# Optimization experiments

Hardware: AMD Instinct MI355X
Metric: run time of the kernel (lower is better)

Reference implementation:

```python
import jax, jax.numpy as jnp
import numpy as np

B, N, E, H, FF = 2, 2048, 1024, 16, 4096
D = E // H  # head dim = 64
LN_EPS = 1e-5


def _layer_norm(x, gamma, beta):
    mu = jnp.mean(x, axis=-1, keepdims=True)
    var = jnp.var(x, axis=-1, keepdims=True)
    return (x - mu) * jax.lax.rsqrt(var + LN_EPS) * gamma + beta


def setup_inputs() -> dict:
    key = jax.random.key(0)
    ks = jax.random.split(key, 12)
    s = 0.02
    return {
        "x": jax.random.normal(ks[0], (B, N, 2), dtype=jnp.float32),
        "W_in": jax.random.normal(ks[1], (2, E), dtype=jnp.float32) * s,
        "b_in": jnp.zeros((E,), dtype=jnp.float32),
        "gamma": jnp.ones((E,), dtype=jnp.float32),
        "beta": jnp.zeros((E,), dtype=jnp.float32),
        "Wq": jax.random.normal(ks[2], (E, E), dtype=jnp.float32) * s,
        "bq": jnp.zeros((E,), dtype=jnp.float32),
        "Wk": jax.random.normal(ks[3], (E, E), dtype=jnp.float32) * s,
        "bk": jnp.zeros((E,), dtype=jnp.float32),
        "Wv": jax.random.normal(ks[4], (E, E), dtype=jnp.float32) * s,
        "bv": jnp.zeros((E,), dtype=jnp.float32),
        "Wo": jax.random.normal(ks[5], (E, E), dtype=jnp.float32) * s,
        "bo": jnp.zeros((E,), dtype=jnp.float32),
        "W1": jax.random.normal(ks[6], (E, FF), dtype=jnp.float32) * s,
        "b1": jnp.zeros((FF,), dtype=jnp.float32),
        "W2": jax.random.normal(ks[7], (FF, E), dtype=jnp.float32) * s,
        "b2": jnp.zeros((E,), dtype=jnp.float32),
    }


def reference(x, W_in, b_in, gamma, beta, Wq, bq, Wk, bk, Wv, bv, Wo, bo, W1, b1, W2, b2):
    # input projection: [B,N,2] -> [B,N,E]
    h = x @ W_in + b_in
    # pre-attention LayerNorm (shared params with pre-FFN LN in original)
    hL = _layer_norm(h, gamma, beta)

    def split_heads(t):  # [B,N,E] -> [B,H,N,D]
        return t.reshape(B, N, H, D).transpose(0, 2, 1, 3)

    q = split_heads(hL @ Wq + bq)
    k = split_heads(hL @ Wk + bk)
    v = split_heads(hL @ Wv + bv)

    # full score matrix, scaled by sqrt(emb_size) as in the original (NOT sqrt(head_dim))
    energy = jnp.einsum("bhqd,bhkd->bhqk", q, k)
    att = jax.nn.softmax(energy / jnp.sqrt(jnp.float32(E)), axis=-1)
    out = jnp.einsum("bhqk,bhkd->bhqd", att, v)
    out = out.transpose(0, 2, 1, 3).reshape(B, N, E)
    out = out @ Wo + bo

    h = h + out  # residual
    # FFN branch with SAME LayerNorm params
    f = _layer_norm(h, gamma, beta)
    f = jax.nn.gelu(f @ W1 + b1, approximate=False)
    f = f @ W2 + b2
    return h + f
```

## Files before the change

### kernel.cpp

```cpp
#include <hip/hip_runtime.h>
#include <hip/hip_bf16.h>
#include <stdint.h>

#define B_  2
#define N_  2048
#define E_  1024
#define H_  16
#define D_  64
#define FF_ 4096
#define M_  (B_ * N_)

typedef __bf16 bf16x8 __attribute__((ext_vector_type(8)));
typedef float  f32x4  __attribute__((ext_vector_type(4)));

__device__ __forceinline__ unsigned short f2bf(float x) {
  union { float f; uint32_t u; } v; v.f = x;
  v.u += 0x7fffu + ((v.u >> 16) & 1u);
  return (unsigned short)(v.u >> 16);
}

__device__ __forceinline__ void async16(void* lds, const void* g) {
  __builtin_amdgcn_global_load_lds(
      (const __attribute__((address_space(1))) uint32_t*)g,
      (__attribute__((address_space(3))) uint32_t*)lds, 16, 0, 0);
}

__global__ __launch_bounds__(256)
void k_transpose_bf16(const float* __restrict__ W, unsigned short* __restrict__ Wt,
                      int K, int N) {
  __shared__ float tile[64][65];
  const int n0 = blockIdx.x * 64, k0 = blockIdx.y * 64;
  const int t = threadIdx.x;
  const int c = t & 63, r4 = t >> 6;
#pragma unroll
  for (int i = 0; i < 16; ++i) {
    int r = r4 + i * 4;
    tile[r][c] = W[(size_t)(k0 + r) * N + n0 + c];
  }
  __syncthreads();
#pragma unroll
  for (int i = 0; i < 16; ++i) {
    int r = r4 + i * 4;
    Wt[(size_t)(n0 + r) * K + k0 + c] = f2bf(tile[c][r]);
  }
}

__global__ __launch_bounds__(256)
void k_inproj_ln(const float* __restrict__ x, const float* __restrict__ Win,
                 const float* __restrict__ bin, const float* __restrict__ gamma,
                 const float* __restrict__ beta, float* __restrict__ h,
                 unsigned short* __restrict__ hL) {
  const int m = blockIdx.x, t = threadIdx.x;
  const float x0 = x[m * 2], x1 = x[m * 2 + 1];
  float hv[4], s = 0.f, s2 = 0.f;
#pragma unroll
  for (int i = 0; i < 4; ++i) {
    int c = t + i * 256;
    float v = x0 * Win[c] + x1 * Win[E_ + c] + bin[c];
    hv[i] = v; s += v; s2 += v * v;
  }
#pragma unroll
  for (int off = 1; off < 64; off <<= 1) { s += __shfl_xor(s, off); s2 += __shfl_xor(s2, off); }
  __shared__ float ws1[4], ws2[4];
  const int w = t >> 6, lane = t & 63;
  if (lane == 0) { ws1[w] = s; ws2[w] = s2; }
  __syncthreads();
  s  = ws1[0] + ws1[1] + ws1[2] + ws1[3];
  s2 = ws2[0] + ws2[1] + ws2[2] + ws2[3];
  const float mu = s * (1.f / E_);
  const float var = s2 * (1.f / E_) - mu * mu;
  const float rs = 1.f / sqrtf(var + 1e-5f);
#pragma unroll
  for (int i = 0; i < 4; ++i) {
    int c = t + i * 256;
    h [(size_t)m * E_ + c] = hv[i];
    hL[(size_t)m * E_ + c] = f2bf((hv[i] - mu) * rs * gamma[c] + beta[c]);
  }
}

__global__ __launch_bounds__(256)
void k_ln(const float* __restrict__ h, const float* __restrict__ gamma,
          const float* __restrict__ beta, unsigned short* __restrict__ o) {
  const int m = blockIdx.x, t = threadIdx.x;
  const float4 v4 = *reinterpret_cast<const float4*>(&h[(size_t)m * E_ + t * 4]);
  float s = v4.x + v4.y + v4.z + v4.w;
  float s2 = v4.x * v4.x + v4.y * v4.y + v4.z * v4.z + v4.w * v4.w;
#pragma unroll
  for (int off = 1; off < 64; off <<= 1) { s += __shfl_xor(s, off); s2 += __shfl_xor(s2, off); }
  __shared__ float ws1[4], ws2[4];
  const int w = t >> 6, lane = t & 63;
  if (lane == 0) { ws1[w] = s; ws2[w] = s2; }
  __syncthreads();
  s  = ws1[0] + ws1[1] + ws1[2] + ws1[3];
  s2 = ws2[0] + ws2[1] + ws2[2] + ws2[3];
  const float mu = s * (1.f / E_);
  const float var = s2 * (1.f / E_) - mu * mu;
  const float rs = 1.f / sqrtf(var + 1e-5f);
  const float vv[4] = {v4.x, v4.y, v4.z, v4.w};
#pragma unroll
  for (int i = 0; i < 4; ++i) {
    int c = t * 4 + i;
    o[(size_t)m * E_ + c] = f2bf((vv[i] - mu) * rs * gamma[c] + beta[c]);
  }
}

template <bool OUT_BF16, bool GELU, bool RES>
__global__ __launch_bounds__(256, 2)
void k_gemm(const unsigned short* __restrict__ A, const unsigned short* __restrict__ Bt,
            const float* __restrict__ bias, const float* __restrict__ res,
            void* __restrict__ Cout, int M, int N, int K) {
  __shared__ unsigned short As[128 * 64];
  __shared__ unsigned short Bs[128 * 64];
  const int t = threadIdx.x, lane = t & 63, w = t >> 6;
  const int wr = w >> 1, wc = w & 1;
  const int row0 = blockIdx.y * 128, col0 = blockIdx.x * 128;
  const int lr = lane & 15, lk = (lane >> 4) * 8;

  f32x4 acc[4][4];
#pragma unroll
  for (int m = 0; m < 4; ++m)
#pragma unroll
    for (int n = 0; n < 4; ++n) acc[m][n] = f32x4{0.f, 0.f, 0.f, 0.f};

  for (int k0 = 0; k0 < K; k0 += 64) {
    __syncthreads();
#pragma unroll
    for (int it = 0; it < 4; ++it) {
      int e = (it * 256 + t) * 8;
      int r = e >> 6, c = e & 63;
      async16(&As[(it * 256 + w * 64) * 8], &A [(size_t)(row0 + r) * K + k0 + c]);
      async16(&Bs[(it * 256 + w * 64) * 8], &Bt[(size_t)(col0 + r) * K + k0 + c]);
    }
    __syncthreads();
#pragma unroll
    for (int ks = 0; ks < 2; ++ks) {
      bf16x8 af[4], bfr[4];
#pragma unroll
      for (int m = 0; m < 4; ++m)
        af[m] = *reinterpret_cast<const bf16x8*>(&As[(wr * 64 + m * 16 + lr) * 64 + ks * 32 + lk]);
#pragma unroll
      for (int n = 0; n < 4; ++n)
        bfr[n] = *reinterpret_cast<const bf16x8*>(&Bs[(wc * 64 + n * 16 + lr) * 64 + ks * 32 + lk]);
#pragma unroll
      for (int m = 0; m < 4; ++m)
#pragma unroll
        for (int n = 0; n < 4; ++n)
          acc[m][n] = __builtin_amdgcn_mfma_f32_16x16x32_bf16(af[m], bfr[n], acc[m][n], 0, 0, 0);
    }
  }
#pragma unroll
  for (int m = 0; m < 4; ++m) {
    const int row_b = row0 + wr * 64 + m * 16 + (lane >> 4) * 4;
#pragma unroll
    for (int n = 0; n < 4; ++n) {
      const int col = col0 + wc * 64 + n * 16 + lr;
      const float bv = bias[col];
#pragma unroll
      for (int r = 0; r < 4; ++r) {
        const int row = row_b + r;
        float v = acc[m][n][r] + bv;
        if (RES) v += res[(size_t)row * N + col];
        if (GELU) v = 0.5f * v * (1.f + erff(v * 0.70710678118f));
        if (OUT_BF16) ((unsigned short*)Cout)[(size_t)row * N + col] = f2bf(v);
        else          ((float*)Cout)[(size_t)row * N + col] = v;
      }
    }
  }
}

__global__ __launch_bounds__(256, 2)
void k_attn(const unsigned short* __restrict__ Q, const unsigned short* __restrict__ K,
            const unsigned short* __restrict__ V, unsigned short* __restrict__ O) {
  __shared__ unsigned short Ks[64 * 64];
  __shared__ unsigned short VT[64 * 64];
  __shared__ unsigned short Ps[4][16 * 64];
  const int t = threadIdx.x, lane = t & 63, w = t >> 6;
  const int qt = blockIdx.x, hh = blockIdx.y, bb = blockIdx.z;
  const int lr = lane & 15, lg = lane >> 4;
  const size_t base = (size_t)bb * N_ * E_ + hh * D_;
  const int q0 = qt * 64 + w * 16;

  bf16x8 qf[2];
#pragma unroll
  for (int ks = 0; ks < 2; ++ks)
    qf[ks] = *reinterpret_cast<const bf16x8*>(&Q[base + (size_t)(q0 + lr) * E_ + ks * 32 + lg * 8]);

  float mrow[4], lrow[4];
  f32x4 oacc[4];
#pragma unroll
  for (int r = 0; r < 4; ++r) { mrow[r] = -1e30f; lrow[r] = 0.f; }
#pragma unroll
  for (int d16 = 0; d16 < 4; ++d16) oacc[d16] = f32x4{0.f, 0.f, 0.f, 0.f};

  for (int kt = 0; kt < N_ / 64; ++kt) {
    __syncthreads();
#pragma unroll
    for (int c2 = 0; c2 < 2; ++c2) {
      int e = (t * 2 + c2) * 8;
      int r = e >> 6, c = e & 63;
      *reinterpret_cast<uint4*>(&Ks[r * 64 + c]) =
          *reinterpret_cast<const uint4*>(&K[base + (size_t)(kt * 64 + r) * E_ + c]);
      uint4 vv = *reinterpret_cast<const uint4*>(&V[base + (size_t)(kt * 64 + r) * E_ + c]);
      const unsigned short* pv = reinterpret_cast<const unsigned short*>(&vv);
#pragma unroll
      for (int j = 0; j < 8; ++j) VT[(c + j) * 64 + r] = pv[j];
    }
    __syncthreads();

    f32x4 sacc[4];
#pragma unroll
    for (int n16 = 0; n16 < 4; ++n16) sacc[n16] = f32x4{0.f, 0.f, 0.f, 0.f};
#pragma unroll
    for (int ks = 0; ks < 2; ++ks)
#pragma unroll
      for (int n16 = 0; n16 < 4; ++n16) {
        bf16x8 kf = *reinterpret_cast<const bf16x8*>(&Ks[(n16 * 16 + lr) * 64 + ks * 32 + lg * 8]);
        sacc[n16] = __builtin_amdgcn_mfma_f32_16x16x32_bf16(qf[ks], kf, sacc[n16], 0, 0, 0);
      }

    float p[4][4];
#pragma unroll
    for (int n16 = 0; n16 < 4; ++n16)
#pragma unroll
      for (int r = 0; r < 4; ++r) p[n16][r] = sacc[n16][r] * 0.03125f;
#pragma unroll
    for (int r = 0; r < 4; ++r) {
      float mx = fmaxf(fmaxf(p[0][r], p[1][r]), fmaxf(p[2][r], p[3][r]));
#pragma unroll
      for (int off = 1; off < 16; off <<= 1) mx = fmaxf(mx, __shfl_xor(mx, off));
      const float mnew = fmaxf(mrow[r], mx);
      const float alpha = expf(mrow[r] - mnew);
      mrow[r] = mnew;
      float ls = 0.f;
#pragma unroll
      for (int n16 = 0; n16 < 4; ++n16) { float pv = expf(p[n16][r] - mnew); p[n16][r] = pv; ls += pv; }
#pragma unroll
      for (int off = 1; off < 16; off <<= 1) ls += __shfl_xor(ls, off);
      lrow[r] = lrow[r] * alpha + ls;
#pragma unroll
      for (int d16 = 0; d16 < 4; ++d16) oacc[d16][r] *= alpha;
    }
#pragma unroll
    for (int n16 = 0; n16 < 4; ++n16)
#pragma unroll
      for (int r = 0; r < 4; ++r)
        Ps[w][(lg * 4 + r) * 64 + n16 * 16 + lr] = f2bf(p[n16][r]);

#pragma unroll
    for (int ks = 0; ks < 2; ++ks) {
      bf16x8 pf = *reinterpret_cast<const bf16x8*>(&Ps[w][lr * 64 + ks * 32 + lg * 8]);
#pragma unroll
      for (int d16 = 0; d16 < 4; ++d16) {
        bf16x8 vf = *reinterpret_cast<const bf16x8*>(&VT[(d16 * 16 + lr) * 64 + ks * 32 + lg * 8]);
        oacc[d16] = __builtin_amdgcn_mfma_f32_16x16x32_bf16(pf, vf, oacc[d16], 0, 0, 0);
      }
    }
  }
#pragma unroll
  for (int r = 0; r < 4; ++r) {
    const float inv = 1.f / lrow[r];
    const size_t rowoff = base + (size_t)(q0 + lg * 4 + r) * E_;
#pragma unroll
    for (int d16 = 0; d16 < 4; ++d16)
      O[rowoff + d16 * 16 + lr] = f2bf(oacc[d16][r] * inv);
  }
}

extern "C" void kernel_launch(void* const* d_in, const int* in_sizes, int n_in,
                              void* d_out, int out_size, void* d_ws, size_t ws_size,
                              hipStream_t stream) {
  (void)in_sizes; (void)n_in; (void)out_size; (void)ws_size;
  const float* x     = (const float*)d_in[0];
  const float* Win   = (const float*)d_in[1];
  const float* bin   = (const float*)d_in[2];
  const float* gamma = (const float*)d_in[3];
  const float* beta  = (const float*)d_in[4];
  const float* Wq    = (const float*)d_in[5];
  const float* bq    = (const float*)d_in[6];
  const float* Wk    = (const float*)d_in[7];
  const float* bk    = (const float*)d_in[8];
  const float* Wv    = (const float*)d_in[9];
  const float* bv    = (const float*)d_in[10];
  const float* Wo    = (const float*)d_in[11];
  const float* bo    = (const float*)d_in[12];
  const float* W1    = (const float*)d_in[13];
  const float* b1    = (const float*)d_in[14];
  const float* W2    = (const float*)d_in[15];
  const float* b2    = (const float*)d_in[16];
  float* out = (float*)d_out;

  char* ws = (char*)d_ws;
  const size_t MB = 1024ull * 1024ull;
  float*          h   = (float*)         (ws + 0);
  float*          h2  = (float*)         (ws + 16 * MB);
  unsigned short* hL  = (unsigned short*)(ws + 32 * MB);
  unsigned short* qb  = (unsigned short*)(ws + 40 * MB);
  unsigned short* kb  = (unsigned short*)(ws + 48 * MB);
  unsigned short* vb  = (unsigned short*)(ws + 56 * MB);
  unsigned short* ao  = (unsigned short*)(ws + 64 * MB);
  unsigned short* f1  = (unsigned short*)(ws + 40 * MB);
  unsigned short* Wqt = (unsigned short*)(ws + 72 * MB);
  unsigned short* Wkt = (unsigned short*)(ws + 74 * MB);
  unsigned short* Wvt = (unsigned short*)(ws + 76 * MB);
  unsigned short* Wot = (unsigned short*)(ws + 78 * MB);
  unsigned short* W1t = (unsigned short*)(ws + 80 * MB);
  unsigned short* W2t = (unsigned short*)(ws + 88 * MB);

  k_transpose_bf16<<<dim3(E_ / 64, E_ / 64), 256, 0, stream>>>(Wq, Wqt, E_, E_);
  k_transpose_bf16<<<dim3(E_ / 64, E_ / 64), 256, 0, stream>>>(Wk, Wkt, E_, E_);
  k_transpose_bf16<<<dim3(E_ / 64, E_ / 64), 256, 0, stream>>>(Wv, Wvt, E_, E_);
  k_transpose_bf16<<<dim3(E_ / 64, E_ / 64), 256, 0, stream>>>(Wo, Wot, E_, E_);
  k_transpose_bf16<<<dim3(FF_ / 64, E_ / 64), 256, 0, stream>>>(W1, W1t, E_, FF_);
  k_transpose_bf16<<<dim3(E_ / 64, FF_ / 64), 256, 0, stream>>>(W2, W2t, FF_, E_);

  k_inproj_ln<<<M_, 256, 0, stream>>>(x, Win, bin, gamma, beta, h, hL);

  k_gemm<true, false, false><<<dim3(E_ / 128, M_ / 128), 256, 0, stream>>>(hL, Wqt, bq, nullptr, qb, M_, E_, E_);
  k_gemm<true, false, false><<<dim3(E_ / 128, M_ / 128), 256, 0, stream>>>(hL, Wkt, bk, nullptr, kb, M_, E_, E_);
  k_gemm<true, false, false><<<dim3(E_ / 128, M_ / 128), 256, 0, stream>>>(hL, Wvt, bv, nullptr, vb, M_, E_, E_);

  k_attn<<<dim3(N_ / 64, H_, B_), 256, 0, stream>>>(qb, kb, vb, ao);

  k_gemm<false, false, true><<<dim3(E_ / 128, M_ / 128), 256, 0, stream>>>(ao, Wot, bo, h, h2, M_, E_, E_);

  k_ln<<<M_, 256, 0, stream>>>(h2, gamma, beta, hL);

  k_gemm<true, true, false><<<dim3(FF_ / 128, M_ / 128), 256, 0, stream>>>(hL, W1t, b1, nullptr, f1, M_, FF_, E_);

  k_gemm<false, false, true><<<dim3(E_ / 128, M_ / 128), 256, 0, stream>>>(f1, W2t, b2, h2, out, M_, E_, FF_);
}
```

Before: 568.6 us.

## Write V transposed from GEMM epilogue and swizzle GEMM blocks across XCDs

The V projection GEMM now writes its output directly in a per-head transposed [B,H,D,N] layout with packed 4-element stores. The attention kernel can then load V^T tiles with vector copies instead of scattering 8 scalar LDS writes per thread. All GEMM launches also remap block indices so consecutive tiles land on the same XCD, aiming for better L2 reuse. A scale parameter is added but is always 1. The V epilogue stores become strided in global memory, which trades some write efficiency for cheaper attention loads.

```diff
diff --git a/kernel.cpp b/kernel.cpp
--- a/kernel.cpp
+++ b/kernel.cpp
@@ -1,6 +1,7 @@
 #include <hip/hip_runtime.h>
 #include <hip/hip_bf16.h>
 #include <stdint.h>
+#include <math.h>
 
 #define B_  2
 #define N_  2048
@@ -12,6 +13,8 @@
 
 typedef __bf16 bf16x8 __attribute__((ext_vector_type(8)));
 typedef float  f32x4  __attribute__((ext_vector_type(4)));
+
+struct __align__(8) us4 { unsigned short v[4]; };
 
 __device__ __forceinline__ unsigned short f2bf(float x) {
   union { float f; uint32_t u; } v; v.f = x;
@@ -104,17 +107,25 @@
   }
 }
 
-template <bool OUT_BF16, bool GELU, bool RES>
+template <int MODE, bool RES>
 __global__ __launch_bounds__(256, 2)
 void k_gemm(const unsigned short* __restrict__ A, const unsigned short* __restrict__ Bt,
             const float* __restrict__ bias, const float* __restrict__ res,
-            void* __restrict__ Cout, int M, int N, int K) {
+            void* __restrict__ Cout, int M, int N, int K, float scale) {
   __shared__ unsigned short As[128 * 64];
   __shared__ unsigned short Bs[128 * 64];
   const int t = threadIdx.x, lane = t & 63, w = t >> 6;
   const int wr = w >> 1, wc = w & 1;
-  const int row0 = blockIdx.y * 128, col0 = blockIdx.x * 128;
-  const int lr = lane & 15, lk = (lane >> 4) * 8;
+
+  const int nwg = gridDim.x * gridDim.y;
+  const int orig = blockIdx.y * gridDim.x + blockIdx.x;
+  const int q = nwg >> 3, r = nwg & 7;
+  const int xcd = orig & 7, idx = orig >> 3;
+  const int swz = (xcd < r ? xcd * (q + 1) : r * (q + 1) + (xcd - r) * q) + idx;
+  const int bx = swz % gridDim.x, by = swz / gridDim.x;
+
+  const int row0 = by * 128, col0 = bx * 128;
+  const int lr = lane & 15, lg = lane >> 4, lk = lg * 8;
 
   f32x4 acc[4][4];
 #pragma unroll
@@ -127,9 +138,9 @@
 #pragma unroll
     for (int it = 0; it < 4; ++it) {
       int e = (it * 256 + t) * 8;
-      int r = e >> 6, c = e & 63;
-      async16(&As[(it * 256 + w * 64) * 8], &A [(size_t)(row0 + r) * K + k0 + c]);
-      async16(&Bs[(it * 256 + w * 64) * 8], &Bt[(size_t)(col0 + r) * K + k0 + c]);
+      int r2 = e >> 6, c = e & 63;
+      async16(&As[(it * 256 + w * 64) * 8], &A [(size_t)(row0 + r2) * K + k0 + c]);
+      async16(&Bs[(it * 256 + w * 64) * 8], &Bt[(size_t)(col0 + r2) * K + k0 + c]);
     }
     __syncthreads();
 #pragma unroll
@@ -150,19 +161,29 @@
   }
 #pragma unroll
   for (int m = 0; m < 4; ++m) {
-    const int row_b = row0 + wr * 64 + m * 16 + (lane >> 4) * 4;
+    const int row_b = row0 + wr * 64 + m * 16 + lg * 4;
 #pragma unroll
     for (int n = 0; n < 4; ++n) {
       const int col = col0 + wc * 64 + n * 16 + lr;
       const float bv = bias[col];
-#pragma unroll
-      for (int r = 0; r < 4; ++r) {
-        const int row = row_b + r;
-        float v = acc[m][n][r] + bv;
-        if (RES) v += res[(size_t)row * N + col];
-        if (GELU) v = 0.5f * v * (1.f + erff(v * 0.70710678118f));
-        if (OUT_BF16) ((unsigned short*)Cout)[(size_t)row * N + col] = f2bf(v);
-        else          ((float*)Cout)[(size_t)row * N + col] = v;
+      if (MODE == 3) {
+        us4 pk;
+#pragma unroll
+        for (int rr = 0; rr < 4; ++rr) pk.v[rr] = f2bf((acc[m][n][rr] + bv) * scale);
+        const int hh = col >> 6, dd = col & 63;
+        const int bb = row_b >> 11, ns = row_b & (N_ - 1);
+        *reinterpret_cast<us4*>(
+            &((unsigned short*)Cout)[((size_t)(bb * H_ + hh) * D_ + dd) * N_ + ns]) = pk;
+      } else {
+#pragma unroll
+        for (int rr = 0; rr < 4; ++rr) {
+          const int row = row_b + rr;
+          float v = (acc[m][n][rr] + bv) * scale;
+          if (RES) v += res[(size_t)row * N + col];
+          if (MODE == 2) v = 0.5f * v * (1.f + erff(v * 0.70710678118f));
+          if (MODE == 0) ((float*)Cout)[(size_t)row * N + col] = v;
+          else           ((unsigned short*)Cout)[(size_t)row * N + col] = f2bf(v);
+        }
       }
     }
   }
@@ -170,7 +191,7 @@
 
 __global__ __launch_bounds__(256, 2)
 void k_attn(const unsigned short* __restrict__ Q, const unsigned short* __restrict__ K,
-            const unsigned short* __restrict__ V, unsigned short* __restrict__ O) {
+            const unsigned short* __restrict__ VTg, unsigned short* __restrict__ O) {
   __shared__ unsigned short Ks[64 * 64];
   __shared__ unsigned short VT[64 * 64];
   __shared__ unsigned short Ps[4][16 * 64];
@@ -178,6 +199,7 @@
   const int qt = blockIdx.x, hh = blockIdx.y, bb = blockIdx.z;
   const int lr = lane & 15, lg = lane >> 4;
   const size_t base = (size_t)bb * N_ * E_ + hh * D_;
+  const size_t vtbase = (size_t)(bb * H_ + hh) * D_ * N_;
   const int q0 = qt * 64 + w * 16;
 
   bf16x8 qf[2];
@@ -196,14 +218,12 @@
     __syncthreads();
 #pragma unroll
     for (int c2 = 0; c2 < 2; ++c2) {
-      int e = (t * 2 + c2) * 8;
-      int r = e >> 6, c = e & 63;
+      const int s = t * 2 + c2;
+      const int r = s >> 3, c = (s & 7) * 8;
       *reinterpret_cast<uint4*>(&Ks[r * 64 + c]) =
           *reinterpret_cast<const uint4*>(&K[base + (size_t)(kt * 64 + r) * E_ + c]);
-      uint4 vv = *reinterpret_cast<const uint4*>(&V[base + (size_t)(kt * 64 + r) * E_ + c]);
-      const unsigned short* pv = reinterpret_cast<const unsigned short*>(&vv);
-#pragma unroll
-      for (int j = 0; j < 8; ++j) VT[(c + j) * 64 + r] = pv[j];
+      *reinterpret_cast<uint4*>(&VT[r * 64 + c]) =
+          *reinterpret_cast<const uint4*>(&VTg[vtbase + (size_t)r * N_ + kt * 64 + c]);
     }
     __syncthreads();
 
@@ -296,7 +316,7 @@
   unsigned short* hL  = (unsigned short*)(ws + 32 * MB);
   unsigned short* qb  = (unsigned short*)(ws + 40 * MB);
   unsigned short* kb  = (unsigned short*)(ws + 48 * MB);
-  unsigned short* vb  = (unsigned short*)(ws + 56 * MB);
+  unsigned short* vt  = (unsigned short*)(ws + 56 * MB);
   unsigned short* ao  = (unsigned short*)(ws + 64 * MB);
   unsigned short* f1  = (unsigned short*)(ws + 40 * MB);
   unsigned short* Wqt = (unsigned short*)(ws + 72 * MB);
@@ -315,17 +335,17 @@
 
   k_inproj_ln<<<M_, 256, 0, stream>>>(x, Win, bin, gamma, beta, h, hL);
 
-  k_gemm<true, false, false><<<dim3(E_ / 128, M_ / 128), 256, 0, stream>>>(hL, Wqt, bq, nullptr, qb, M_, E_, E_);
-  k_gemm<true, false, false><<<dim3(E_ / 128, M_ / 128), 256, 0, stream>>>(hL, Wkt, bk, nullptr, kb, M_, E_, E_);
-  k_gemm<true, false, false><<<dim3(E_ / 128, M_ / 128), 256, 0, stream>>>(hL, Wvt, bv, nullptr, vb, M_, E_, E_);
-
-  k_attn<<<dim3(N_ / 64, H_, B_), 256, 0, stream>>>(qb, kb, vb, ao);
-
-  k_gemm<false, false, true><<<dim3(E_ / 128, M_ / 128), 256, 0, stream>>>(ao, Wot, bo, h, h2, M_, E_, E_);
+  k_gemm<1, false><<<dim3(E_ / 128, M_ / 128), 256, 0, stream>>>(hL, Wqt, bq, nullptr, qb, M_, E_, E_, 1.f);
+  k_gemm<1, false><<<dim3(E_ / 128, M_ / 128), 256, 0, stream>>>(hL, Wkt, bk, nullptr, kb, M_, E_, E_, 1.f);
+  k_gemm<3, false><<<dim3(E_ / 128, M_ / 128), 256, 0, stream>>>(hL, Wvt, bv, nullptr, vt, M_, E_, E_, 1.f);
+
+  k_attn<<<dim3(N_ / 64, H_, B_), 256, 0, stream>>>(qb, kb, vt, ao);
+
+  k_gemm<0, true><<<dim3(E_ / 128, M_ / 128), 256, 0, stream>>>(ao, Wot, bo, h, h2, M_, E_, E_, 1.f);
 
   k_ln<<<M_, 256, 0, stream>>>(h2, gamma, beta, hL);
 
-  k_gemm<true, true, false><<<dim3(FF_ / 128, M_ / 128), 256, 0, stream>>>(hL, W1t, b1, nullptr, f1, M_, FF_, E_);
-
-  k_gemm<false, false, true><<<dim3(E_ / 128, M_ / 128), 256, 0, stream>>>(f1, W2t, b2, h2, out, M_, E_, FF_);
-}
+  k_gemm<2, false><<<dim3(FF_ / 128, M_ / 128), 256, 0, stream>>>(hL, W1t, b1, nullptr, f1, M_, FF_, E_, 1.f);
+
+  k_gemm<0, true><<<dim3(E_ / 128, M_ / 128), 256, 0, stream>>>(f1, W2t, b2, h2, out, M_, E_, FF_, 1.f);
+}
```

Result: faster. 548.3 us (-3.6%).
